# Optimization experiments

Measured on AMD Instinct MI355X. Metric: run time of the kernel, lower is better.

## Reference

```python
import jax, jax.numpy as jnp
import numpy as np

B, D, K = 512, 128, 131072
TEMP = 0.07
PTR = 0  # queue_ptr starts at 0; B <= K so single contiguous write


def _normalize(x, axis):
    return x / jnp.linalg.norm(x, axis=axis, keepdims=True)


def setup_inputs() -> dict:
    key = jax.random.key(0)
    k = jax.random.split(key, 7)
    return {
        "predict0": jax.random.normal(k[0], (B, D), jnp.float32),
        "predict1": jax.random.normal(k[1], (B, D), jnp.float32),
        "project0": jax.random.normal(k[2], (B, D), jnp.float32),
        "project1": jax.random.normal(k[3], (B, D), jnp.float32),
        "queue": jax.random.normal(k[4], (D, K), jnp.float32),
        "queue_id": jax.random.randint(k[5], (K,), 0, 100000, jnp.int64) if jax.config.jax_enable_x64 else jax.random.randint(k[5], (K,), 0, 100000, jnp.int32),
        "ids": jax.random.randint(k[6], (B,), 0, 100000, jnp.int64) if jax.config.jax_enable_x64 else jax.random.randint(k[6], (B,), 0, 100000, jnp.int32),
    }


def _find_nn(proj, queue_n, queue_id, ids):
    # [B, K] similarity, mask out entries with same sample id, argmax, gather cols
    sim = proj @ queue_n                                   # [B, K]
    is_own = queue_id[None, :] == ids[:, None]             # [B, K]
    sim = jnp.where(is_own, jnp.float32(-1.0), sim)
    idx = jnp.argmax(sim, axis=1)                          # [B]
    return queue_n[:, idx]                                 # [D, B]


def _nnclr_loss(predicted, nn, temperature):
    # logits[i, j] = nn_i . predicted_j / T ; labels = arange(B)
    logits = (nn.T @ predicted.T) / temperature            # [B, B]
    logp = jax.nn.log_softmax(logits, axis=-1)
    return -jnp.mean(jnp.diagonal(logp))


def reference(predict0, predict1, project0, project1, queue, queue_id, ids):
    # forward_encoder's normalization (encoder itself is external and modeled out)
    p0 = _normalize(predict0, 1)
    p1 = _normalize(predict1, 1)
    z0 = _normalize(project0, 1)
    z1 = _normalize(project1, 1)
    queue_n = _normalize(queue, 0)  # queue stored normalized along dim 0

    # find_nn / queue are no_grad in the original
    nn0 = jax.lax.stop_gradient(_find_nn(jax.lax.stop_gradient(z0), queue_n, queue_id, ids))
    nn1 = jax.lax.stop_gradient(_find_nn(jax.lax.stop_gradient(z1), queue_n, queue_id, ids))

    loss0 = _nnclr_loss(p0, nn1, TEMP)
    loss1 = _nnclr_loss(p1, nn0, TEMP)
    loss = (loss0 + loss1) * 0.5

    # _dequeue_and_enqueue: ptr=0, B <= K -> contiguous slice write
    new_queue = jax.lax.dynamic_update_slice(queue_n, jax.lax.stop_gradient(z0.T), (0, PTR))
    new_queue_id = jax.lax.dynamic_update_slice(queue_id, ids, (PTR,))
    new_ptr = jnp.array((PTR + B) % K, dtype=queue_id.dtype)
    return loss, new_queue, new_queue_id, new_ptr
```

## Files before the change

### kernel.cpp

```cpp
#include <hip/hip_runtime.h>
#include <hip/hip_bf16.h>

typedef _Float16 half8 __attribute__((ext_vector_type(8)));
typedef _Float16 half4 __attribute__((ext_vector_type(4)));
typedef float f32x4 __attribute__((ext_vector_type(4)));

#define B 512
#define D 128
#define K 131072
#define TEMP 0.07f
#define NKB 256
#define KT_PER 32
#define NSS 16

#define INVN_OFF 0
#define Z0_OFF   131072
#define Z1_OFF   196608
#define P0_OFF   262144
#define P1_OFF   327680
#define ZF16_OFF 393216
#define QA_OFF   458752
#define PVAL_OFF 8847360
#define IDX_OFF  9373696
#define LP_OFF   9374720
#define IDM_OFF  9375744

__device__ __forceinline__ void gload_lds16(const _Float16* g, _Float16* l) {
  __builtin_amdgcn_global_load_lds(
      (const __attribute__((address_space(1))) unsigned int*)g,
      (__attribute__((address_space(3))) unsigned int*)l, 16, 0, 0);
}

__global__ __launch_bounds__(128) void rownorm_k(
    const float* __restrict__ p0, const float* __restrict__ p1,
    const float* __restrict__ z0, const float* __restrict__ z1,
    float* __restrict__ w, _Float16* __restrict__ zf16) {
  int row = blockIdx.x & (B - 1);
  int which = blockIdx.x >> 9;
  const float* src; float* dst;
  switch (which) {
    case 0: src = z0; dst = w + Z0_OFF; break;
    case 1: src = z1; dst = w + Z1_OFF; break;
    case 2: src = p0; dst = w + P0_OFF; break;
    default: src = p1; dst = w + P1_OFF; break;
  }
  int tid = threadIdx.x;
  float v = src[row * D + tid];
  float s = v * v;
  #pragma unroll
  for (int o = 32; o; o >>= 1) s += __shfl_xor(s, o);
  __shared__ float sm[2];
  if ((tid & 63) == 0) sm[tid >> 6] = s;
  __syncthreads();
  float inv = rsqrtf(sm[0] + sm[1]);
  float nv = v * inv;
  dst[row * D + tid] = nv;
  if (which < 2) zf16[(which * B + row) * D + tid] = (_Float16)nv;
}

__global__ __launch_bounds__(256) void idmask_k(
    const int* __restrict__ qid, const int* __restrict__ ids,
    unsigned short* __restrict__ idm) {
  __shared__ int sids[B];
  int tid = threadIdx.x;
  sids[tid] = ids[tid];
  sids[tid + 256] = ids[tid + 256];
  __syncthreads();
  int k = blockIdx.x * 256 + tid;
  int myq = qid[k];
  bool match = false;
  #pragma unroll 4
  for (int j = 0; j < B; j += 4) {
    int4 i4 = *(const int4*)&sids[j];
    match |= (myq == i4.x) | (myq == i4.y) | (myq == i4.z) | (myq == i4.w);
  }
  unsigned long long bal = __ballot(match);
  int lane = tid & 63;
  if ((lane & 15) == 0)
    idm[k >> 4] = (unsigned short)((bal >> lane) & 0xFFFFull);
}

__global__ __launch_bounds__(256) void colq_k(
    const float* __restrict__ q, const int* __restrict__ qid,
    const int* __restrict__ ids, const float* __restrict__ w_z0,
    float* __restrict__ invn, float* __restrict__ out,
    _Float16* __restrict__ qA) {
  __shared__ float psum[8][128];
  __shared__ float invs[128];
  __shared__ float sm2[2];
  __shared__ float fcol[128];
  __shared__ _Float16 tile[128][136];
  int tid = threadIdx.x;
  int kb = blockIdx.x;
  int k0 = kb * 128;
  int kc = tid & 31, dg = tid >> 5;

  float fqv = 0.f;
  if (kb > 4 && tid < 128) fqv = q[(size_t)tid * K + (k0 - 1)];

  float4 v[16];
  {
    float4 acc = {0.f, 0.f, 0.f, 0.f};
    #pragma unroll
    for (int i = 0; i < 16; i++) {
      int d = dg * 16 + i;
      v[i] = *(const float4*)(q + (size_t)d * K + k0 + kc * 4);
      acc.x = fmaf(v[i].x, v[i].x, acc.x); acc.y = fmaf(v[i].y, v[i].y, acc.y);
      acc.z = fmaf(v[i].z, v[i].z, acc.z); acc.w = fmaf(v[i].w, v[i].w, acc.w);
    }
    *(float4*)&psum[dg][kc * 4] = acc;
  }
  __syncthreads();
  if (tid < 128) {
    float s = 0.f;
    #pragma unroll
    for (int g2 = 0; g2 < 8; g2++) s += psum[g2][tid];
    float inv = rsqrtf(s);
    invs[tid] = inv;
    invn[k0 + tid] = inv;
    int kk = k0 + tid;
    out[1 + (size_t)D * K + kk] = (float)((kk < B) ? ids[kk] : qid[kk]);
  }
  if (kb > 4 && tid < 128) {
    float s2 = fqv * fqv;
    #pragma unroll
    for (int o = 32; o; o >>= 1) s2 += __shfl_xor(s2, o);
    if ((tid & 63) == 0) sm2[tid >> 6] = s2;
  }
  __syncthreads();
  if (kb > 4) {
    if (tid < 128) fcol[tid] = fqv * rsqrtf(sm2[0] + sm2[1]);
  } else if (kb == 4) {
    if (tid < 32)
      *(float4*)&fcol[tid * 4] = *(const float4*)(w_z0 + (size_t)511 * D + tid * 4);
  }
  __syncthreads();

  float4 iv = *(const float4*)&invs[kc * 4];
  if (kb >= 4) {
    #pragma unroll
    for (int i = 0; i < 16; i++) {
      int d = dg * 16 + i;
      float o0 = v[i].x * iv.x, o1 = v[i].y * iv.y;
      float o2 = v[i].z * iv.z, o3 = v[i].w * iv.w;
      half4 t = {(_Float16)o0, (_Float16)o1, (_Float16)o2, (_Float16)o3};
      *(half4*)&tile[d][kc * 4] = t;
      float p3 = __shfl_up(o3, 1);
      float x0 = (kc == 0) ? fcol[d] : p3;
      float4 st = {x0, o0, o1, o2};
      *(float4*)(out + (size_t)d * K + k0 + kc * 4) = st;
      if (kb == 1023 && kc == 31)
        out[1 + (size_t)d * K + (K - 1)] = o3;
    }
  } else {
    #pragma unroll
    for (int i = 0; i < 16; i++) {
      int d = dg * 16 + i;
      float o0 = v[i].x * iv.x, o1 = v[i].y * iv.y;
      float o2 = v[i].z * iv.z, o3 = v[i].w * iv.w;
      half4 t = {(_Float16)o0, (_Float16)o1, (_Float16)o2, (_Float16)o3};
      *(half4*)&tile[d][kc * 4] = t;
      float* oc = out + 1 + (size_t)d * K + k0 + kc * 4;
      int col = k0 + kc * 4;
      oc[0] = w_z0[(size_t)(col + 0) * D + d];
      oc[1] = w_z0[(size_t)(col + 1) * D + d];
      oc[2] = w_z0[(size_t)(col + 2) * D + d];
      oc[3] = w_z0[(size_t)(col + 3) * D + d];
    }
  }
  __syncthreads();
  {
    int dc = tid >> 6, l = tid & 63;
    int g = l >> 4, c = l & 15;
    #pragma unroll
    for (int kt = 0; kt < 8; kt++) {
      half8 f;
      #pragma unroll
      for (int i = 0; i < 8; i++) {
        int d = g * 4 + (i & 3) + ((i >> 2) << 4) + dc * 32;
        f[i] = tile[d][kt * 16 + c];
      }
      int ktg = kb * 8 + kt;
      *(half8*)(qA + (size_t)((ktg * 4 + dc) * 64 + l) * 8) = f;
    }
  }
}

#define PROCESS(AF, Q4) do { \
  _Pragma("unroll") \
  for (int nt = 0; nt < 4; nt++) { \
    f32x4 acc = {0.f, 0.f, 0.f, 0.f}; \
    _Pragma("unroll") \
    for (int dc = 0; dc < 4; dc++) \
      acc = __builtin_amdgcn_mfma_f32_16x16x32_f16(AF[dc], bf[nt][dc], acc, 0, 0, 0); \
    _Pragma("unroll") \
    for (int r = 0; r < 4; r++) { \
      int qv_ = (r == 0) ? Q4.x : (r == 1) ? Q4.y : (r == 2) ? Q4.z : Q4.w; \
      float sm_ = (qv_ == myid[nt]) ? -1.0f : acc[r]; \
      best[nt] = fmaxf(best[nt], sm_); \
    } \
  } \
} while (0)

#define PROCESS_CLEAN(AF) do { \
  _Pragma("unroll") \
  for (int nt = 0; nt < 4; nt++) { \
    f32x4 acc = {0.f, 0.f, 0.f, 0.f}; \
    _Pragma("unroll") \
    for (int dc = 0; dc < 4; dc++) \
      acc = __builtin_amdgcn_mfma_f32_16x16x32_f16(AF[dc], bf[nt][dc], acc, 0, 0, 0); \
    best[nt] = fmaxf(best[nt], \
        fmaxf(fmaxf(acc[0], acc[1]), fmaxf(acc[2], acc[3]))); \
  } \
} while (0)

__global__ __launch_bounds__(256) void nnsearch_k(
    const _Float16* __restrict__ qA, const _Float16* __restrict__ zf16,
    const int* __restrict__ qid, const int* __restrict__ ids,
    const unsigned short* __restrict__ idm, float* __restrict__ pval) {
  __shared__ __align__(16) _Float16 qtile[3][2][2048];
  __shared__ __align__(16) int qid_lds[512];
  __shared__ unsigned short qmask_lds[32];
  int tid = threadIdx.x;
  int flat = blockIdx.x;
  int cls = flat & 7;
  int kb = cls * 32 + (flat >> 5);
  int rg = (flat >> 3) & 3;
  int wave = tid >> 6, lane = tid & 63;
  int g = lane >> 4, c = lane & 15;
  int rowbase = rg * 256 + wave * 64;
  int kt0 = kb * KT_PER;

  #pragma unroll
  for (int j = 0; j < 2; j++)
    gload_lds16(qA + (size_t)(((kt0 + j) * 4 + wave) * 64 + lane) * 8,
                &qtile[0][j][wave * 512]);
  #pragma unroll
  for (int j = 0; j < 2; j++)
    gload_lds16(qA + (size_t)(((kt0 + 2 + j) * 4 + wave) * 64 + lane) * 8,
                &qtile[1][j][wave * 512]);
  qid_lds[tid] = qid[kb * 512 + tid];
  qid_lds[tid + 256] = qid[kb * 512 + tid + 256];
  if (tid < 32) qmask_lds[tid] = idm[kt0 + tid];

  half8 bf[4][4];
  int myid[4];
  #pragma unroll
  for (int nt = 0; nt < 4; nt++) {
    int row = rowbase + nt * 16 + c;
    myid[nt] = ids[row & (B - 1)];
    #pragma unroll
    for (int dc = 0; dc < 4; dc++) {
      const _Float16* zr = zf16 + row * D + dc * 32 + g * 4;
      half4 lo = *(const half4*)zr;
      half4 hi = *(const half4*)(zr + 16);
      half8 f = {lo[0], lo[1], lo[2], lo[3], hi[0], hi[1], hi[2], hi[3]};
      bf[nt][dc] = f;
    }
  }
  __syncthreads();

  float best[4] = {-2.f, -2.f, -2.f, -2.f};
  int cur = 0;
  for (int s = 0; s < NSS; s++) {
    half8 af0[4], af1[4];
    #pragma unroll
    for (int dc = 0; dc < 4; dc++)
      af0[dc] = *(const half8*)&qtile[cur][0][dc * 512 + lane * 8];
    #pragma unroll
    for (int dc = 0; dc < 4; dc++)
      af1[dc] = *(const half8*)&qtile[cur][1][dc * 512 + lane * 8];
    int ma = qmask_lds[s * 2 + 0];
    int mb = qmask_lds[s * 2 + 1];
    if (s + 2 < NSS) {
      int nbuf = cur + 2; if (nbuf >= 3) nbuf -= 3;
      #pragma unroll
      for (int j = 0; j < 2; j++)
        gload_lds16(qA + (size_t)(((kt0 + (s + 2) * 2 + j) * 4 + wave) * 64 + lane) * 8,
                    &qtile[nbuf][j][wave * 512]);
    }
    __builtin_amdgcn_s_setprio(1);
    if (ma) {
      int4 q4a = *(const int4*)&qid_lds[(s * 2 + 0) * 16 + g * 4];
      PROCESS(af0, q4a);
    } else {
      PROCESS_CLEAN(af0);
    }
    if (mb) {
      int4 q4b = *(const int4*)&qid_lds[(s * 2 + 1) * 16 + g * 4];
      PROCESS(af1, q4b);
    } else {
      PROCESS_CLEAN(af1);
    }
    __builtin_amdgcn_s_setprio(0);
    if (s < NSS - 1) {
      asm volatile("s_waitcnt lgkmcnt(0)" ::: "memory");
      if (s + 2 < NSS) asm volatile("s_waitcnt vmcnt(2)" ::: "memory");
      else             asm volatile("s_waitcnt vmcnt(0)" ::: "memory");
      __builtin_amdgcn_sched_barrier(0);
      __builtin_amdgcn_s_barrier();
      __builtin_amdgcn_sched_barrier(0);
    }
    cur += 1; if (cur >= 3) cur -= 3;
  }

  #pragma unroll
  for (int nt = 0; nt < 4; nt++) {
    float v = best[nt];
    v = fmaxf(v, __shfl_xor(v, 16));
    v = fmaxf(v, __shfl_xor(v, 32));
    if (g == 0) {
      int row = rowbase + nt * 16 + c;
      pval[row * NKB + kb] = v;
    }
  }
}

__global__ __launch_bounds__(256) void nnpick_k(
    const float* __restrict__ pval, const _Float16* __restrict__ qA,
    const _Float16* __restrict__ zf16, const int* __restrict__ qid,
    const int* __restrict__ ids, int* __restrict__ idxout) {
  int row = blockIdx.x;
  int tid = threadIdx.x;
  int wave = tid >> 6, lane = tid & 63;
  int g = lane >> 4;
  __shared__ unsigned sv[4];
  __shared__ unsigned skb[4];
  __shared__ int s_kb;
  __shared__ float s_wv;
  {
    float a = pval[row * NKB + tid];
    unsigned v = (__float_as_uint(fmaf(a, 0.5f, 3.0f)) << 9) | (unsigned)(NKB - 1 - tid);
    #pragma unroll
    for (int o = 32; o; o >>= 1) {
      unsigned ov = __shfl_xor(v, o);
      v = v > ov ? v : ov;
    }
    if (lane == 0) sv[wave] = v;
  }
  __syncthreads();
  if (tid == 0) {
    unsigned v = sv[0];
    #pragma unroll
    for (int wv = 1; wv < 4; wv++) v = v > sv[wv] ? v : sv[wv];
    int kbw = (NKB - 1) - (int)(v & 0x1FFu);
    s_kb = kbw;
    s_wv = pval[row * NKB + kbw];
  }
  __syncthreads();
  int kb = s_kb;
  float wv = s_wv;
  int myid = ids[row & (B - 1)];

  half8 bf[4];
  #pragma unroll
  for (int dc = 0; dc < 4; dc++) {
    const _Float16* zr = zf16 + row * D + dc * 32 + g * 4;
    half4 lo = *(const half4*)zr;
    half4 hi = *(const half4*)(zr + 16);
    half8 f = {lo[0], lo[1], lo[2], lo[3], hi[0], hi[1], hi[2], hi[3]};
    bf[dc] = f;
  }

  unsigned kbest = 0x7FFFFFFFu;
  int ktbase = kb * KT_PER + wave * 8;
  for (int kt = 0; kt < 8; kt++) {
    int ktg = ktbase + kt;
    half8 af[4];
    #pragma unroll
    for (int dc = 0; dc < 4; dc++)
      af[dc] = *(const half8*)(qA + (size_t)((ktg * 4 + dc) * 64 + lane) * 8);
    int4 q4 = *(const int4*)(qid + ktg * 16 + g * 4);
    f32x4 acc = {0.f, 0.f, 0.f, 0.f};
    #pragma unroll
    for (int dc = 0; dc < 4; dc++)
      acc = __builtin_amdgcn_mfma_f32_16x16x32_f16(af[dc], bf[dc], acc, 0, 0, 0);
    #pragma unroll
    for (int r = 0; r < 4; r++) {
      int qv = (r == 0) ? q4.x : (r == 1) ? q4.y : (r == 2) ? q4.z : q4.w;
      float sm = (qv == myid) ? -1.0f : acc[r];
      if (sm == wv) {
        unsigned kk = (unsigned)(ktg * 16 + g * 4 + r);
        kbest = kbest < kk ? kbest : kk;
      }
    }
  }
  unsigned o1 = __shfl_xor(kbest, 16); kbest = kbest < o1 ? kbest : o1;
  unsigned o2 = __shfl_xor(kbest, 32); kbest = kbest < o2 ? kbest : o2;
  if (lane == 0) skb[wave] = kbest;
  __syncthreads();
  if (tid == 0) {
    unsigned v = skb[0];
    #pragma unroll
    for (int wv2 = 1; wv2 < 4; wv2++) v = v < skb[wv2] ? v : skb[wv2];
    idxout[row] = (int)(v < (K - 1) ? v : (K - 1));
  }
}

__global__ __launch_bounds__(256) void loss_k(
    const float* __restrict__ q, const float* __restrict__ invn,
    const int* __restrict__ idxout, const float* __restrict__ w,
    float* __restrict__ lpart) {
  int i0 = blockIdx.x * 8;
  int v = blockIdx.y;
  int tid = threadIdx.x;
  __shared__ float nns[8][D];
  __shared__ float rm[8][4], re[8][4], sdlds[8];
  #pragma unroll
  for (int ii = 0; ii < 4; ii++) {
    int i = ii * 2 + (tid >> 7);
    int d = tid & 127;
    int nnidx = idxout[(v ? 0 : B) + i0 + i];
    nns[i][d] = q[(size_t)d * K + nnidx] * invn[nnidx];
  }
  __syncthreads();
  const float* pr = w + (v ? P1_OFF : P0_OFF);
  const float* r0 = pr + tid * D;
  const float* r1 = pr + (tid + 256) * D;
  float a0[8] = {0, 0, 0, 0, 0, 0, 0, 0};
  float a1[8] = {0, 0, 0, 0, 0, 0, 0, 0};
  for (int d = 0; d < D; d += 4) {
    float4 x0 = *(const float4*)(r0 + d);
    float4 x1 = *(const float4*)(r1 + d);
    #pragma unroll
    for (int i = 0; i < 8; i++) {
      float4 n = *(const float4*)&nns[i][d];
      a0[i] = fmaf(x0.x, n.x, a0[i]); a0[i] = fmaf(x0.y, n.y, a0[i]);
      a0[i] = fmaf(x0.z, n.z, a0[i]); a0[i] = fmaf(x0.w, n.w, a0[i]);
      a1[i] = fmaf(x1.x, n.x, a1[i]); a1[i] = fmaf(x1.y, n.y, a1[i]);
      a1[i] = fmaf(x1.z, n.z, a1[i]); a1[i] = fmaf(x1.w, n.w, a1[i]);
    }
  }
  #pragma unroll
  for (int i = 0; i < 8; i++) {
    a0[i] *= (1.0f / TEMP);
    a1[i] *= (1.0f / TEMP);
  }
  #pragma unroll
  for (int i = 0; i < 8; i++) {
    int ig = i0 + i;
    if ((ig & 256) == 0) { if (tid == ig) sdlds[i] = a0[i]; }
    else { if (tid == (ig & 255)) sdlds[i] = a1[i]; }
  }
  int wv = tid >> 6;
  #pragma unroll
  for (int i = 0; i < 8; i++) {
    float m = fmaxf(a0[i], a1[i]);
    #pragma unroll
    for (int o = 32; o; o >>= 1) m = fmaxf(m, __shfl_xor(m, o));
    if ((tid & 63) == 0) rm[i][wv] = m;
  }
  __syncthreads();
  #pragma unroll
  for (int i = 0; i < 8; i++) {
    float m = fmaxf(fmaxf(rm[i][0], rm[i][1]), fmaxf(rm[i][2], rm[i][3]));
    float e = expf(a0[i] - m) + expf(a1[i] - m);
    #pragma unroll
    for (int o = 32; o; o >>= 1) e += __shfl_xor(e, o);
    if ((tid & 63) == 0) re[i][wv] = e;
  }
  __syncthreads();
  if (tid < 8) {
    int i = tid;
    float m = fmaxf(fmaxf(rm[i][0], rm[i][1]), fmaxf(rm[i][2], rm[i][3]));
    float s = re[i][0] + re[i][1] + re[i][2] + re[i][3];
    lpart[v * B + i0 + i] = sdlds[i] - m - logf(s);
  }
}

__global__ __launch_bounds__(256) void final_k(
    const float* __restrict__ lpart, float* __restrict__ out) {
  int tid = threadIdx.x;
  float s = lpart[tid] + lpart[tid + 256] + lpart[tid + 512] + lpart[tid + 768];
  #pragma unroll
  for (int o = 32; o; o >>= 1) s += __shfl_xor(s, o);
  __shared__ float sm[4];
  if ((tid & 63) == 0) sm[tid >> 6] = s;
  __syncthreads();
  if (tid == 0) {
    float total = sm[0] + sm[1] + sm[2] + sm[3];
    out[0] = -total * (1.0f / 1024.0f);
    out[1 + D * K + K] = 512.0f;
  }
}

extern "C" void kernel_launch(void* const* d_in, const int* in_sizes, int n_in,
                              void* d_out, int out_size, void* d_ws, size_t ws_size,
                              hipStream_t stream) {
  const float* p0 = (const float*)d_in[0];
  const float* p1 = (const float*)d_in[1];
  const float* z0 = (const float*)d_in[2];
  const float* z1 = (const float*)d_in[3];
  const float* q  = (const float*)d_in[4];
  const int* qid  = (const int*)d_in[5];
  const int* ids  = (const int*)d_in[6];
  float* out = (float*)d_out;
  float* w = (float*)d_ws;
  float* invn = w + INVN_OFF;
  _Float16* zf16 = (_Float16*)(w + ZF16_OFF);
  _Float16* qA   = (_Float16*)(w + QA_OFF);
  float* pval = w + PVAL_OFF;
  int* idxout = (int*)(w + IDX_OFF);
  float* lpart = w + LP_OFF;
  unsigned short* idm = (unsigned short*)(w + IDM_OFF);

  rownorm_k<<<2048, 128, 0, stream>>>(p0, p1, z0, z1, w, zf16);
  idmask_k<<<K / 256, 256, 0, stream>>>(qid, ids, idm);
  colq_k<<<K / 128, 256, 0, stream>>>(q, qid, ids, w + Z0_OFF, invn, out, qA);
  nnsearch_k<<<1024, 256, 0, stream>>>(qA, zf16, qid, ids, idm, pval);
  nnpick_k<<<1024, 256, 0, stream>>>(pval, qA, zf16, qid, ids, idxout);
  dim3 gl(B / 8, 2);
  loss_k<<<gl, 256, 0, stream>>>(q, invn, idxout, w, lpart);
  final_k<<<1, 256, 0, stream>>>(lpart, out);
}
```

Baseline: 120.2 us.

## Give each wave a private LDS triple buffer and drop block barriers in NN search

```diff
diff --git a/kernel.cpp b/kernel.cpp
--- a/kernel.cpp
+++ b/kernel.cpp
@@ -11,7 +11,6 @@
 #define TEMP 0.07f
 #define NKB 256
 #define KT_PER 32
-#define NSS 16
 
 #define INVN_OFF 0
 #define Z0_OFF   131072
@@ -218,7 +217,7 @@
     const _Float16* __restrict__ qA, const _Float16* __restrict__ zf16,
     const int* __restrict__ qid, const int* __restrict__ ids,
     const unsigned short* __restrict__ idm, float* __restrict__ pval) {
-  __shared__ __align__(16) _Float16 qtile[3][2][2048];
+  __shared__ __align__(16) _Float16 qtile[4][3][2048];
   __shared__ __align__(16) int qid_lds[512];
   __shared__ unsigned short qmask_lds[32];
   int tid = threadIdx.x;
@@ -233,12 +232,10 @@
 
   #pragma unroll
   for (int j = 0; j < 2; j++)
-    gload_lds16(qA + (size_t)(((kt0 + j) * 4 + wave) * 64 + lane) * 8,
-                &qtile[0][j][wave * 512]);
-  #pragma unroll
-  for (int j = 0; j < 2; j++)
-    gload_lds16(qA + (size_t)(((kt0 + 2 + j) * 4 + wave) * 64 + lane) * 8,
-                &qtile[1][j][wave * 512]);
+    #pragma unroll
+    for (int dc = 0; dc < 4; dc++)
+      gload_lds16(qA + (size_t)(((kt0 + j) * 4 + dc) * 64 + lane) * 8,
+                  &qtile[wave][j][dc * 512]);
   qid_lds[tid] = qid[kb * 512 + tid];
   qid_lds[tid + 256] = qid[kb * 512 + tid + 256];
   if (tid < 32) qmask_lds[tid] = idm[kt0 + tid];
@@ -261,47 +258,32 @@
   __syncthreads();
 
   float best[4] = {-2.f, -2.f, -2.f, -2.f};
-  int cur = 0;
-  for (int s = 0; s < NSS; s++) {
-    half8 af0[4], af1[4];
+  for (int kt = 0; kt < KT_PER; kt++) {
+    int cur = kt; if (cur >= 3) cur -= 3 * ((unsigned)(cur * 0x5556) >> 16);
+    const _Float16* rb = &qtile[wave][cur][0];
+    if (kt < KT_PER - 1) { asm volatile("s_waitcnt vmcnt(4)" ::: "memory"); }
+    else                 { asm volatile("s_waitcnt vmcnt(0)" ::: "memory"); }
+    __builtin_amdgcn_sched_barrier(0);
+    half8 af[4];
     #pragma unroll
     for (int dc = 0; dc < 4; dc++)
-      af0[dc] = *(const half8*)&qtile[cur][0][dc * 512 + lane * 8];
-    #pragma unroll
-    for (int dc = 0; dc < 4; dc++)
-      af1[dc] = *(const half8*)&qtile[cur][1][dc * 512 + lane * 8];
-    int ma = qmask_lds[s * 2 + 0];
-    int mb = qmask_lds[s * 2 + 1];
-    if (s + 2 < NSS) {
-      int nbuf = cur + 2; if (nbuf >= 3) nbuf -= 3;
+      af[dc] = *(const half8*)(rb + dc * 512 + lane * 8);
+    if (kt + 2 < KT_PER) {
+      int nb = cur + 2; if (nb >= 3) nb -= 3;
       #pragma unroll
-      for (int j = 0; j < 2; j++)
-        gload_lds16(qA + (size_t)(((kt0 + (s + 2) * 2 + j) * 4 + wave) * 64 + lane) * 8,
-                    &qtile[nbuf][j][wave * 512]);
-    }
+      for (int dc = 0; dc < 4; dc++)
+        gload_lds16(qA + (size_t)(((kt0 + kt + 2) * 4 + dc) * 64 + lane) * 8,
+                    &qtile[wave][nb][dc * 512]);
+    }
+    int ma = qmask_lds[kt];
     __builtin_amdgcn_s_setprio(1);
     if (ma) {
-      int4 q4a = *(const int4*)&qid_lds[(s * 2 + 0) * 16 + g * 4];
-      PROCESS(af0, q4a);
+      int4 q4 = *(const int4*)&qid_lds[kt * 16 + g * 4];
+      PROCESS(af, q4);
     } else {
-      PROCESS_CLEAN(af0);
-    }
-    if (mb) {
-      int4 q4b = *(const int4*)&qid_lds[(s * 2 + 1) * 16 + g * 4];
-      PROCESS(af1, q4b);
-    } else {
-      PROCESS_CLEAN(af1);
+      PROCESS_CLEAN(af);
     }
     __builtin_amdgcn_s_setprio(0);
-    if (s < NSS - 1) {
-      asm volatile("s_waitcnt lgkmcnt(0)" ::: "memory");
-      if (s + 2 < NSS) asm volatile("s_waitcnt vmcnt(2)" ::: "memory");
-      else             asm volatile("s_waitcnt vmcnt(0)" ::: "memory");
-      __builtin_amdgcn_sched_barrier(0);
-      __builtin_amdgcn_s_barrier();
-      __builtin_amdgcn_sched_barrier(0);
-    }
-    cur += 1; if (cur >= 3) cur -= 3;
   }
 
   #pragma unroll
```

New measurement: 130.4 us. 1.08x slower.
